# Kernel optimization log

Measured on AMD Instinct MI355X. Metric: run time of the kernel, lower is better.

Reference implementation:

```python
import jax, jax.numpy as jnp
import numpy as np

B, S, D_IN = 2, 2048, 1024
H, DA, DH = 16, 64, 64          # num_heads, attention_dim, head_dim (linear_hidden_dim)
EMBED = 1024
KSIZE = 1


def causal_conv1d(x_bsc, w):
    """x_bsc: (B,S,Cin); w: (Cout,Cin,K). Left-pad K-1 -> causal. Returns (B,Cout,S)."""
    k = w.shape[-1]
    x_bcs = jnp.transpose(x_bsc, (0, 2, 1))
    x_bcs = jnp.pad(x_bcs, ((0, 0), (0, 0), (k - 1, 0)))
    return jax.lax.conv_general_dilated(
        x_bcs, w, window_strides=(1,), padding='VALID',
        dimension_numbers=('NCH', 'OIH', 'NCH'))


def setup_inputs() -> dict:
    key = jax.random.key(0)
    ks = jax.random.split(key, 7)
    x = jax.random.normal(ks[0], (B, S, D_IN), dtype=jnp.float32)
    # causal mask: 1 where attended, 0 where masked (masked_fill where ==0)
    attn_mask = jnp.tril(jnp.ones((S, S), dtype=jnp.int32))[None, None]  # (1,1,S,S)
    wq = 0.02 * jax.random.normal(ks[1], (H * DA, D_IN, KSIZE), dtype=jnp.float32)
    wk = 0.02 * jax.random.normal(ks[2], (H * DA, D_IN, KSIZE), dtype=jnp.float32)
    wv = 0.02 * jax.random.normal(ks[3], (H * DH, D_IN, KSIZE), dtype=jnp.float32)
    w_out = 0.02 * jax.random.normal(ks[4], (EMBED, H * DH), dtype=jnp.float32)
    b_out = 0.02 * jax.random.normal(ks[5], (EMBED,), dtype=jnp.float32)
    return {"x": x, "attn_mask": attn_mask, "wq": wq, "wk": wk, "wv": wv,
            "w_out": w_out, "b_out": b_out}


def reference(x, attn_mask, wq, wk, wv, w_out, b_out):
    b, s, _ = x.shape
    scale = DH ** (-0.5)  # NOTE: torch code scales by head_dim, not attention_dim
    q = causal_conv1d(x, wq)  # (B, H*DA, S)
    k = causal_conv1d(x, wk)  # (B, H*DA, S)
    v = causal_conv1d(x, wv)  # (B, H*DH, S)
    q = q.reshape(b, H, DA, s).transpose(0, 1, 3, 2)  # (B,H,S,DA)
    k = k.reshape(b, H, DA, s).transpose(0, 1, 3, 2)
    v = v.reshape(b, H, DH, s).transpose(0, 1, 3, 2)  # (B,H,S,DH)
    scores = scale * jnp.einsum('bhnd,bhmd->bhnm', q, k)
    scores = jnp.where(attn_mask == 0, -jnp.inf, scores)
    probs = jax.nn.softmax(scores, axis=-1)
    context = jnp.einsum('bhnm,bhmd->bhnd', probs, v)  # (B,H,S,DH)
    context = context.transpose(0, 2, 1, 3).reshape(b, s, H * DH)
    return context @ w_out.T + b_out
```

## Files before the change

kernel.cpp:

```cpp
#include <hip/hip_runtime.h>
#include <math.h>


typedef __bf16 bf16;
typedef __bf16 bf16x8 __attribute__((ext_vector_type(8)));
typedef __bf16 bf16x4 __attribute__((ext_vector_type(4)));
typedef float  f32x4  __attribute__((ext_vector_type(4)));

#define MFMA16(a, b, c) __builtin_amdgcn_mfma_f32_16x16x32_bf16((a), (b), (c), 0, 0, 0)

__device__ __forceinline__ void gll16(const void* g, void* l) {
    __builtin_amdgcn_global_load_lds(
        (__attribute__((address_space(1))) unsigned int*)g,
        (__attribute__((address_space(3))) unsigned int*)l, 16, 0, 0);
}

__global__ __launch_bounds__(256) void cvt_all_kernel(
    const float* __restrict__ x,  const float* __restrict__ wq,
    const float* __restrict__ wk, const float* __restrict__ wv,
    const float* __restrict__ wo,
    bf16* __restrict__ xb,  bf16* __restrict__ wqb, bf16* __restrict__ wkb,
    bf16* __restrict__ wvb, bf16* __restrict__ wob)
{
    #pragma unroll
    for (int k = 0; k < 4; k++) {
        const int blk = blockIdx.x * 4 + k;
        const float* src; bf16* dst; int off; float scale = 1.f;
        if (blk < 4096)      { src = x;  dst = xb;  off = blk * 1024; }
        else if (blk < 5120) { src = wq; dst = wqb; off = (blk - 4096) * 1024;
                               scale = 0.18033688011112042f; }
        else if (blk < 6144) { src = wk; dst = wkb; off = (blk - 5120) * 1024; }
        else if (blk < 7168) { src = wv; dst = wvb; off = (blk - 6144) * 1024; }
        else                 { src = wo; dst = wob; off = (blk - 7168) * 1024; }
        const int i = off + threadIdx.x * 4;
        f32x4 v = *(const f32x4*)(src + i);
        bf16x4 o;
        o[0] = (bf16)(v[0] * scale); o[1] = (bf16)(v[1] * scale);
        o[2] = (bf16)(v[2] * scale); o[3] = (bf16)(v[3] * scale);
        *(bf16x4*)(dst + i) = o;
    }
}

__global__ __launch_bounds__(256, 3) void qkv_mfma_kernel(
    const bf16* __restrict__ xb, const bf16* __restrict__ wqb,
    const bf16* __restrict__ wkb, const bf16* __restrict__ wvb,
    bf16* __restrict__ Qb, bf16* __restrict__ Kb, bf16* __restrict__ Vtb)
{
    __shared__ bf16 As[2][128 * 32];
    __shared__ bf16 Bs[2][128 * 32];
    const int lin = blockIdx.x + 32 * blockIdx.y;
    const int xcd = lin & 7, lid = lin >> 3;
    const int rem = xcd * 96 + lid;
    const int mt = rem & 31;
    const int nt = rem >> 5;
    const int which = nt >> 3;
    const bf16* Wm = (which == 0) ? wqb : (which == 1) ? wkb : wvb;

    const int t = threadIdx.x;
    const int w = t >> 6, lane = t & 63, quad = lane >> 4, l16 = lane & 15;
    const int wm = (w >> 1) * 64, wn = (w & 1) * 64;
    const int srow = lane >> 2;
    const int scol = ((lane & 3) ^ ((lane >> 3) & 3)) * 8;
    const int gx = (l16 >> 1) & 3;

    const bf16* Ab = xb + ((size_t)(mt * 128) + srow) * 1024;
    const bf16* Bb = Wm + ((size_t)((nt & 7) * 128) + srow) * 1024;

    f32x4 acc[4][4];
    #pragma unroll
    for (int i = 0; i < 4; i++)
        #pragma unroll
        for (int j = 0; j < 4; j++)
            #pragma unroll
            for (int r = 0; r < 4; r++) acc[i][j][r] = 0.f;

    gll16(Ab + (size_t)(w * 16) * 1024 + scol,       As[0] + w * 512);
    gll16(Ab + (size_t)((w + 4) * 16) * 1024 + scol, As[0] + (w + 4) * 512);
    gll16(Bb + (size_t)(w * 16) * 1024 + scol,       Bs[0] + w * 512);
    gll16(Bb + (size_t)((w + 4) * 16) * 1024 + scol, Bs[0] + (w + 4) * 512);

    for (int it = 0; it < 32; it++) {
        const int cur = it & 1, nxt = cur ^ 1;
        __syncthreads();
        if (it < 31) {
            const int kn = it * 32 + 32;
            gll16(Ab + (size_t)(w * 16) * 1024 + kn + scol,       As[nxt] + w * 512);
            gll16(Ab + (size_t)((w + 4) * 16) * 1024 + kn + scol, As[nxt] + (w + 4) * 512);
            gll16(Bb + (size_t)(w * 16) * 1024 + kn + scol,       Bs[nxt] + w * 512);
            gll16(Bb + (size_t)((w + 4) * 16) * 1024 + kn + scol, Bs[nxt] + (w + 4) * 512);
        }
        bf16x8 af[4], bfr[4];
        #pragma unroll
        for (int i = 0; i < 4; i++)
            af[i] = *(const bf16x8*)&As[cur][(wm + i * 16 + l16) * 32 +
                                             (quad ^ gx) * 8];
        #pragma unroll
        for (int j = 0; j < 4; j++)
            bfr[j] = *(const bf16x8*)&Bs[cur][(wn + j * 16 + l16) * 32 +
                                              (quad ^ gx) * 8];
        #pragma unroll
        for (int i = 0; i < 4; i++)
            #pragma unroll
            for (int j = 0; j < 4; j++)
                acc[i][j] = MFMA16(af[i], bfr[j], acc[i][j]);
    }

    const int nbase = (nt & 7) * 128 + wn;
    if (which == 2) {
        #pragma unroll
        for (int i = 0; i < 4; i++) {
            const int m0 = mt * 128 + wm + i * 16 + quad * 4;
            const int bb = m0 >> 11, s0 = m0 & 2047;
            #pragma unroll
            for (int j = 0; j < 4; j++) {
                const int n = nbase + j * 16 + l16;
                const int h = n >> 6, d = n & 63;
                bf16x4 pk;
                #pragma unroll
                for (int r = 0; r < 4; r++) pk[r] = (bf16)acc[i][j][r];
                *(bf16x4*)&Vtb[(((size_t)(bb * 16 + h)) * 64 + d) * 2048 + s0] = pk;
            }
        }
    } else {
        bf16* Out = (which == 0) ? Qb : Kb;
        #pragma unroll
        for (int i = 0; i < 4; i++) {
            #pragma unroll
            for (int r = 0; r < 4; r++) {
                const int m = mt * 128 + wm + i * 16 + quad * 4 + r;
                const int bb = m >> 11, s = m & 2047;
                #pragma unroll
                for (int j = 0; j < 4; j++) {
                    const int n = nbase + j * 16 + l16;
                    const int h = n >> 6, d = n & 63;
                    Out[(((size_t)(bb * 16 + h)) * 2048 + s) * 64 + d] =
                        (bf16)acc[i][j][r];
                }
            }
        }
    }
}

__global__ __launch_bounds__(256, 2) void attn_mfma_kernel(
    const bf16* __restrict__ Qb, const bf16* __restrict__ Kb,
    const bf16* __restrict__ Vtb, bf16* __restrict__ ctxb)
{
    __shared__ bf16 Ks[2][128 * 64];
    __shared__ bf16 Vts[2][64 * 128];
    __shared__ bf16 Pl[4][16 * 128];

    const int id = blockIdx.x;
    const int bh = id & 31;
    const int pr = id >> 5;
    const int qa = pr, qb = 31 - pr;
    const int h = bh & 15, b = bh >> 4;
    const int t = threadIdx.x;
    const int w = t >> 6, lane = t & 63, quad = lane >> 4, l16 = lane & 15;

    const size_t hb = (size_t)(b * 16 + h);
    const bf16* Qh = Qb + hb * (2048 * 64);
    const bf16* Kh = Kb + hb * (2048 * 64);
    const bf16* Vh = Vtb + hb * (64 * 2048);

    bf16x8 qf0[2], qf1[2];
    {
        const bf16* Qr0 = Qh + (size_t)(qa * 64 + w * 16 + l16) * 64;
        qf0[0] = *(const bf16x8*)(Qr0 + quad * 8);
        qf0[1] = *(const bf16x8*)(Qr0 + 32 + quad * 8);
        const bf16* Qr1 = Qh + (size_t)(qb * 64 + w * 16 + l16) * 64;
        qf1[0] = *(const bf16x8*)(Qr1 + quad * 8);
        qf1[1] = *(const bf16x8*)(Qr1 + 32 + quad * 8);
    }

    bf16x8 ones;
    #pragma unroll
    for (int i = 0; i < 8; i++) ones[i] = (bf16)1.0f;

    f32x4 o0[4], o1[4], l0, l1;
    #pragma unroll
    for (int r = 0; r < 4; r++) { l0[r] = 0.f; l1[r] = 0.f; }
    #pragma unroll
    for (int dt = 0; dt < 4; dt++)
        #pragma unroll
        for (int r = 0; r < 4; r++) { o0[dt][r] = 0.f; o1[dt][r] = 0.f; }

    const int ksr = lane >> 3, ksc = lane & 7;
    const int vsr = lane >> 4, vsc = lane & 15;

    #define STAGE(ktv, buf)                                                   \
        {                                                                     \
            _Pragma("unroll")                                                 \
            for (int j = 0; j < 4; j++) {                                     \
                const int c = 4 * w + j;                                      \
                const int kr = c * 8 + ksr;                                   \
                gll16(Kh + (size_t)((ktv) * 128 + kr) * 64 +                  \
                          ((ksc ^ (kr & 7)) * 8),                             \
                      Ks[buf] + c * 512);                                     \
                const int vr = c * 4 + vsr;                                   \
                gll16(Vh + (size_t)vr * 2048 + (ktv) * 128 +                  \
                          ((vsc ^ (vr & 15)) * 8),                            \
                      Vts[buf] + c * 512);                                    \
            }                                                                 \
        }

    #define ITER(qt64, ktv, diag, qfv, oacc, lacc, cur)                       \
        {                                                                     \
            f32x4 sacc[8];                                                    \
            __builtin_amdgcn_s_setprio(1);                                    \
            _Pragma("unroll")                                                 \
            for (int tt = 0; tt < 8; tt++) {                                  \
                _Pragma("unroll")                                             \
                for (int r = 0; r < 4; r++) sacc[tt][r] = 0.f;                \
                const int krow = tt * 16 + l16;                               \
                bf16x8 kf0 = *(const bf16x8*)&Ks[cur][krow * 64 +             \
                                 ((quad)     ^ (krow & 7)) * 8];              \
                bf16x8 kf1 = *(const bf16x8*)&Ks[cur][krow * 64 +             \
                                 ((quad + 4) ^ (krow & 7)) * 8];              \
                sacc[tt] = MFMA16(kf0, (qfv)[0], sacc[tt]);                   \
                sacc[tt] = MFMA16(kf1, (qfv)[1], sacc[tt]);                   \
            }                                                                 \
            __builtin_amdgcn_s_setprio(0);                                    \
            const int qrow = (qt64) * 64 + w * 16 + l16;                      \
            _Pragma("unroll")                                                 \
            for (int tt = 0; tt < 8; tt++) {                                  \
                bf16x4 pk;                                                    \
                _Pragma("unroll")                                             \
                for (int r = 0; r < 4; r++) {                                 \
                    float p = __builtin_amdgcn_exp2f(sacc[tt][r]);            \
                    if ((diag) && ((ktv) * 128 + tt * 16 + quad * 4 + r) > qrow) \
                        p = 0.f;                                              \
                    pk[r] = (bf16)p;                                          \
                }                                                             \
                const int cs = (tt * 2 + (quad >> 1)) ^ l16;                  \
                *(bf16x4*)&Pl[w][l16 * 128 + cs * 8 + (quad & 1) * 4] = pk;   \
            }                                                                 \
            bf16x8 ap[4];                                                     \
            __builtin_amdgcn_s_setprio(1);                                    \
            _Pragma("unroll")                                                 \
            for (int u = 0; u < 4; u++) {                                     \
                ap[u] = *(const bf16x8*)&Pl[w][l16 * 128 +                    \
                             ((quad + 4 * u) ^ l16) * 8];                     \
                (lacc) = MFMA16(ap[u], ones, (lacc));                         \
            }                                                                 \
            _Pragma("unroll")                                                 \
            for (int dt = 0; dt < 4; dt++) {                                  \
                const int drow = dt * 16 + l16;                               \
                _Pragma("unroll")                                             \
                for (int u = 0; u < 4; u++) {                                 \
                    bf16x8 bv = *(const bf16x8*)&Vts[cur][drow * 128 +        \
                                     ((4 * u + quad) ^ (drow & 15)) * 8];     \
                    (oacc)[dt] = MFMA16(ap[u], bv, (oacc)[dt]);               \
                }                                                             \
            }                                                                 \
            __builtin_amdgcn_s_setprio(0);                                    \
        }

    const int na = (qa >> 1) + 1;
    STAGE(0, 0);

    for (int v = 0; v < 17; v++) {
        const int cur = v & 1, nxt = cur ^ 1;
        __syncthreads();
        if (v < 16) {
            const int vn = v + 1;
            const int ktn = (vn < na) ? vn : vn - na;
            STAGE(ktn, nxt);
        }
        if (v < na) {
            ITER(qa, v, (v == na - 1), qf0, o0, l0, cur);
        } else {
            const int kt = v - na;
            ITER(qb, kt, (v == 16), qf1, o1, l1, cur);
        }
    }
    #undef STAGE
    #undef ITER

    #pragma unroll
    for (int r = 0; r < 4; r++) {
        const float inv0 = 1.f / l0[r];
        const int s0 = qa * 64 + w * 16 + quad * 4 + r;
        const float inv1 = 1.f / l1[r];
        const int s1 = qb * 64 + w * 16 + quad * 4 + r;
        #pragma unroll
        for (int dt = 0; dt < 4; dt++) {
            ctxb[((size_t)(b * 2048 + s0)) * 1024 + h * 64 + dt * 16 + l16] =
                (bf16)(o0[dt][r] * inv0);
            ctxb[((size_t)(b * 2048 + s1)) * 1024 + h * 64 + dt * 16 + l16] =
                (bf16)(o1[dt][r] * inv1);
        }
    }
}

__global__ __launch_bounds__(256, 3) void oproj_mfma_kernel(
    const bf16* __restrict__ ctxb, const bf16* __restrict__ wob,
    const float* __restrict__ b_out, float* __restrict__ out)
{
    __shared__ bf16 As[2][64 * 64];
    __shared__ bf16 Bs[2][128 * 64];
    const int mt = blockIdx.x;
    const int nt = blockIdx.y;
    const int t = threadIdx.x;
    const int w = t >> 6, lane = t & 63, quad = lane >> 4, l16 = lane & 15;
    const int srow8 = lane >> 3;
    const int scg = ((lane & 7) ^ srow8) * 8;

    const int wrow = (w >> 1) * 32;
    const int wcol = (w & 1) * 64;

    const bf16* Ab = ctxb + (size_t)(mt * 64) * 1024;
    const bf16* Bb = wob + (size_t)(nt * 128) * 1024;

    f32x4 acc[2][4];
    #pragma unroll
    for (int i = 0; i < 2; i++)
        #pragma unroll
        for (int j = 0; j < 4; j++)
            #pragma unroll
            for (int r = 0; r < 4; r++) acc[i][j][r] = 0.f;

    #define OSTG(buf, kk)                                                     \
        {                                                                     \
            gll16(Ab + (size_t)(w * 8 + srow8) * 1024 + (kk) + scg,           \
                  As[buf] + w * 512);                                         \
            gll16(Ab + (size_t)((w + 4) * 8 + srow8) * 1024 + (kk) + scg,     \
                  As[buf] + (w + 4) * 512);                                   \
            _Pragma("unroll")                                                 \
            for (int c = 0; c < 4; c++) {                                     \
                const int ch = w + 4 * c;                                     \
                gll16(Bb + (size_t)(ch * 8 + srow8) * 1024 + (kk) + scg,      \
                      Bs[buf] + ch * 512);                                    \
            }                                                                 \
        }

    OSTG(0, 0);

    for (int it = 0; it < 16; it++) {
        const int cur = it & 1, nxt = cur ^ 1;
        __syncthreads();
        if (it < 15) { OSTG(nxt, it * 64 + 64); }
        bf16x8 af[2][2], bfv[4][2];
        #pragma unroll
        for (int i = 0; i < 2; i++) {
            const int ro = wrow + i * 16 + l16;
            af[i][0] = *(const bf16x8*)&As[cur][ro * 64 + ((quad)     ^ (ro & 7)) * 8];
            af[i][1] = *(const bf16x8*)&As[cur][ro * 64 + ((quad + 4) ^ (ro & 7)) * 8];
        }
        #pragma unroll
        for (int j = 0; j < 4; j++) {
            const int ro = wcol + j * 16 + l16;
            bfv[j][0] = *(const bf16x8*)&Bs[cur][ro * 64 + ((quad)     ^ (ro & 7)) * 8];
            bfv[j][1] = *(const bf16x8*)&Bs[cur][ro * 64 + ((quad + 4) ^ (ro & 7)) * 8];
        }
        #pragma unroll
        for (int i = 0; i < 2; i++)
            #pragma unroll
            for (int j = 0; j < 4; j++) {
                acc[i][j] = MFMA16(af[i][0], bfv[j][0], acc[i][j]);
                acc[i][j] = MFMA16(af[i][1], bfv[j][1], acc[i][j]);
            }
    }
    #undef OSTG

    #pragma unroll
    for (int i = 0; i < 2; i++)
        #pragma unroll
        for (int j = 0; j < 4; j++)
            #pragma unroll
            for (int r = 0; r < 4; r++) {
                const int m = mt * 64 + wrow + i * 16 + quad * 4 + r;
                const int n = nt * 128 + wcol + j * 16 + l16;
                out[(size_t)m * 1024 + n] = acc[i][j][r] + b_out[n];
            }
}

extern "C" void kernel_launch(void* const* d_in, const int* in_sizes, int n_in,
                              void* d_out, int out_size, void* d_ws, size_t ws_size,
                              hipStream_t stream)
{
    const float* x     = (const float*)d_in[0];
    const float* wq    = (const float*)d_in[2];
    const float* wk    = (const float*)d_in[3];
    const float* wv    = (const float*)d_in[4];
    const float* w_out = (const float*)d_in[5];
    const float* b_out = (const float*)d_in[6];
    float* out = (float*)d_out;

    char* ws = (char*)d_ws;
    bf16* xb   = (bf16*)(ws);
    bf16* wqb  = (bf16*)(ws + (8u  << 20));
    bf16* wkb  = (bf16*)(ws + (10u << 20));
    bf16* wvb  = (bf16*)(ws + (12u << 20));
    bf16* wob  = (bf16*)(ws + (14u << 20));
    bf16* Qb   = (bf16*)(ws + (16u << 20));
    bf16* Kb   = (bf16*)(ws + (24u << 20));
    bf16* Vtb  = (bf16*)(ws + (32u << 20));
    bf16* ctxb = (bf16*)(ws + (40u << 20));

    cvt_all_kernel<<<2048, 256, 0, stream>>>(x, wq, wk, wv, w_out,
                                             xb, wqb, wkb, wvb, wob);
    qkv_mfma_kernel<<<dim3(32, 24), 256, 0, stream>>>(xb, wqb, wkb, wvb, Qb, Kb, Vtb);
    attn_mfma_kernel<<<512, 256, 0, stream>>>(Qb, Kb, Vtb, ctxb);
    oproj_mfma_kernel<<<dim3(64, 8), 256, 0, stream>>>(ctxb, wob, b_out, out);
}
```

Baseline: 178.4 us.

## Rework attention with 32x32 MFMA, register-resident P, and per-tile causal scheduling

The attention kernel moves from 16x16x32 to 32x32x16 bf16 MFMA. Each wave now owns 32 query rows, and each block owns one 128-row query tile. The softmax probabilities are packed with v_cvt_pk_bf16 and rearranged across lanes with v_permlane32_swap, so they stay in registers instead of going through a shared-memory scratch buffer. Row sums become scalar adds plus one cross-half shuffle, replacing the MFMA against a ones vector. The old pairing of a short and a long query tile in one block is dropped. Load balance now relies on launch order, with the second half of the grid running tiles in reverse. That can leave tail imbalance and adds register pressure from the 16-wide accumulators.

Result: no change. 177.5 us, median of 2 (-0.5%).

```diff
diff --git a/kernel.cpp b/kernel.cpp
--- a/kernel.cpp
+++ b/kernel.cpp
@@ -6,13 +6,21 @@
 typedef __bf16 bf16x8 __attribute__((ext_vector_type(8)));
 typedef __bf16 bf16x4 __attribute__((ext_vector_type(4)));
 typedef float  f32x4  __attribute__((ext_vector_type(4)));
+typedef float  f32x16 __attribute__((ext_vector_type(16)));
 
 #define MFMA16(a, b, c) __builtin_amdgcn_mfma_f32_16x16x32_bf16((a), (b), (c), 0, 0, 0)
+#define MFMA32(a, b, c) __builtin_amdgcn_mfma_f32_32x32x16_bf16((a), (b), (c), 0, 0, 0)
 
 __device__ __forceinline__ void gll16(const void* g, void* l) {
     __builtin_amdgcn_global_load_lds(
         (__attribute__((address_space(1))) unsigned int*)g,
         (__attribute__((address_space(3))) unsigned int*)l, 16, 0, 0);
+}
+
+__device__ __forceinline__ unsigned int cvt_pk_bf16(float lo, float hi) {
+    unsigned int r;
+    asm("v_cvt_pk_bf16_f32 %0, %1, %2" : "=v"(r) : "v"(lo), "v"(hi));
+    return r;
 }
 
 __global__ __launch_bounds__(256) void cvt_all_kernel(
@@ -147,42 +155,33 @@
 {
     __shared__ bf16 Ks[2][128 * 64];
     __shared__ bf16 Vts[2][64 * 128];
-    __shared__ bf16 Pl[4][16 * 128];
-
-    const int id = blockIdx.x;
-    const int bh = id & 31;
-    const int pr = id >> 5;
-    const int qa = pr, qb = 31 - pr;
+
+    const int g = blockIdx.x;
+    const int base = g & 255;
+    const int bh = base & 31;
+    const int tp = base >> 5;
+    const int t  = (g < 256) ? tp : 15 - tp;
     const int h = bh & 15, b = bh >> 4;
-    const int t = threadIdx.x;
-    const int w = t >> 6, lane = t & 63, quad = lane >> 4, l16 = lane & 15;
+    const int tid = threadIdx.x;
+    const int w = tid >> 6, lane = tid & 63;
+    const int l32 = lane & 31, hv = lane >> 5;
 
     const size_t hb = (size_t)(b * 16 + h);
     const bf16* Qh = Qb + hb * (2048 * 64);
     const bf16* Kh = Kb + hb * (2048 * 64);
     const bf16* Vh = Vtb + hb * (64 * 2048);
 
-    bf16x8 qf0[2], qf1[2];
-    {
-        const bf16* Qr0 = Qh + (size_t)(qa * 64 + w * 16 + l16) * 64;
-        qf0[0] = *(const bf16x8*)(Qr0 + quad * 8);
-        qf0[1] = *(const bf16x8*)(Qr0 + 32 + quad * 8);
-        const bf16* Qr1 = Qh + (size_t)(qb * 64 + w * 16 + l16) * 64;
-        qf1[0] = *(const bf16x8*)(Qr1 + quad * 8);
-        qf1[1] = *(const bf16x8*)(Qr1 + 32 + quad * 8);
-    }
-
-    bf16x8 ones;
-    #pragma unroll
-    for (int i = 0; i < 8; i++) ones[i] = (bf16)1.0f;
-
-    f32x4 o0[4], o1[4], l0, l1;
-    #pragma unroll
-    for (int r = 0; r < 4; r++) { l0[r] = 0.f; l1[r] = 0.f; }
-    #pragma unroll
-    for (int dt = 0; dt < 4; dt++)
-        #pragma unroll
-        for (int r = 0; r < 4; r++) { o0[dt][r] = 0.f; o1[dt][r] = 0.f; }
+    const int qrow = t * 128 + w * 32 + l32;
+
+    bf16x8 qf[4];
+    #pragma unroll
+    for (int ks = 0; ks < 4; ks++)
+        qf[ks] = *(const bf16x8*)(Qh + (size_t)qrow * 64 + ks * 16 + hv * 8);
+
+    f32x16 o0, o1, zero16;
+    #pragma unroll
+    for (int r = 0; r < 16; r++) { o0[r] = 0.f; o1[r] = 0.f; zero16[r] = 0.f; }
+    float lacc = 0.f;
 
     const int ksr = lane >> 3, ksc = lane & 7;
     const int vsr = lane >> 4, vsc = lane & 15;
@@ -203,92 +202,81 @@
             }                                                                 \
         }
 
-    #define ITER(qt64, ktv, diag, qfv, oacc, lacc, cur)                       \
-        {                                                                     \
-            f32x4 sacc[8];                                                    \
-            __builtin_amdgcn_s_setprio(1);                                    \
-            _Pragma("unroll")                                                 \
-            for (int tt = 0; tt < 8; tt++) {                                  \
-                _Pragma("unroll")                                             \
-                for (int r = 0; r < 4; r++) sacc[tt][r] = 0.f;                \
-                const int krow = tt * 16 + l16;                               \
-                bf16x8 kf0 = *(const bf16x8*)&Ks[cur][krow * 64 +             \
-                                 ((quad)     ^ (krow & 7)) * 8];              \
-                bf16x8 kf1 = *(const bf16x8*)&Ks[cur][krow * 64 +             \
-                                 ((quad + 4) ^ (krow & 7)) * 8];              \
-                sacc[tt] = MFMA16(kf0, (qfv)[0], sacc[tt]);                   \
-                sacc[tt] = MFMA16(kf1, (qfv)[1], sacc[tt]);                   \
-            }                                                                 \
-            __builtin_amdgcn_s_setprio(0);                                    \
-            const int qrow = (qt64) * 64 + w * 16 + l16;                      \
-            _Pragma("unroll")                                                 \
-            for (int tt = 0; tt < 8; tt++) {                                  \
-                bf16x4 pk;                                                    \
-                _Pragma("unroll")                                             \
-                for (int r = 0; r < 4; r++) {                                 \
-                    float p = __builtin_amdgcn_exp2f(sacc[tt][r]);            \
-                    if ((diag) && ((ktv) * 128 + tt * 16 + quad * 4 + r) > qrow) \
-                        p = 0.f;                                              \
-                    pk[r] = (bf16)p;                                          \
-                }                                                             \
-                const int cs = (tt * 2 + (quad >> 1)) ^ l16;                  \
-                *(bf16x4*)&Pl[w][l16 * 128 + cs * 8 + (quad & 1) * 4] = pk;   \
-            }                                                                 \
-            bf16x8 ap[4];                                                     \
-            __builtin_amdgcn_s_setprio(1);                                    \
-            _Pragma("unroll")                                                 \
-            for (int u = 0; u < 4; u++) {                                     \
-                ap[u] = *(const bf16x8*)&Pl[w][l16 * 128 +                    \
-                             ((quad + 4 * u) ^ l16) * 8];                     \
-                (lacc) = MFMA16(ap[u], ones, (lacc));                         \
-            }                                                                 \
-            _Pragma("unroll")                                                 \
-            for (int dt = 0; dt < 4; dt++) {                                  \
-                const int drow = dt * 16 + l16;                               \
-                _Pragma("unroll")                                             \
-                for (int u = 0; u < 4; u++) {                                 \
-                    bf16x8 bv = *(const bf16x8*)&Vts[cur][drow * 128 +        \
-                                     ((4 * u + quad) ^ (drow & 15)) * 8];     \
-                    (oacc)[dt] = MFMA16(ap[u], bv, (oacc)[dt]);               \
-                }                                                             \
-            }                                                                 \
-            __builtin_amdgcn_s_setprio(0);                                    \
-        }
-
-    const int na = (qa >> 1) + 1;
     STAGE(0, 0);
 
-    for (int v = 0; v < 17; v++) {
-        const int cur = v & 1, nxt = cur ^ 1;
+    for (int v = 0; v <= t; v++) {
+        const int cur = v & 1;
         __syncthreads();
-        if (v < 16) {
-            const int vn = v + 1;
-            const int ktn = (vn < na) ? vn : vn - na;
-            STAGE(ktn, nxt);
-        }
-        if (v < na) {
-            ITER(qa, v, (v == na - 1), qf0, o0, l0, cur);
-        } else {
-            const int kt = v - na;
-            ITER(qb, kt, (v == 16), qf1, o1, l1, cur);
-        }
+        if (v < t) STAGE(v + 1, cur ^ 1);
+        const bool diag = (v == t);
+
+        f32x16 sacc[4];
+        const int rowx = l32 & 7;
+        __builtin_amdgcn_s_setprio(1);
+        #pragma unroll
+        for (int c = 0; c < 4; c++) {
+            const int key = c * 32 + l32;
+            bf16x8 kf0 = *(const bf16x8*)&Ks[cur][key * 64 + ((hv ^ rowx) * 8)];
+            sacc[c] = MFMA32(kf0, qf[0], zero16);
+            #pragma unroll
+            for (int ks = 1; ks < 4; ks++) {
+                bf16x8 kf = *(const bf16x8*)&Ks[cur][key * 64 +
+                                (((ks * 2 + hv) ^ rowx) * 8)];
+                sacc[c] = MFMA32(kf, qf[ks], sacc[c]);
+            }
+        }
+        __builtin_amdgcn_s_setprio(0);
+
+        #pragma unroll
+        for (int c = 0; c < 4; c++) {
+            #pragma unroll
+            for (int r = 0; r < 16; r++) {
+                float p = __builtin_amdgcn_exp2f(sacc[c][r]);
+                if (diag) {
+                    const int key = v * 128 + c * 32 + (r & 3) + 8 * (r >> 2)
+                                    + 4 * hv;
+                    if (key > qrow) p = 0.f;
+                }
+                sacc[c][r] = p;
+                lacc += p;
+            }
+        }
+
+        __builtin_amdgcn_s_setprio(1);
+        #pragma unroll
+        for (int c = 0; c < 4; c++) {
+            #pragma unroll
+            for (int hh = 0; hh < 2; hh++) {
+                unsigned int W0 = cvt_pk_bf16(sacc[c][8 * hh + 0], sacc[c][8 * hh + 1]);
+                unsigned int W1 = cvt_pk_bf16(sacc[c][8 * hh + 2], sacc[c][8 * hh + 3]);
+                unsigned int W2 = cvt_pk_bf16(sacc[c][8 * hh + 4], sacc[c][8 * hh + 5]);
+                unsigned int W3 = cvt_pk_bf16(sacc[c][8 * hh + 6], sacc[c][8 * hh + 7]);
+                asm volatile("v_permlane32_swap_b32 %0, %1" : "+v"(W0), "+v"(W2));
+                asm volatile("v_permlane32_swap_b32 %0, %1" : "+v"(W1), "+v"(W3));
+                union { unsigned int u[4]; bf16x8 v8; } fu;
+                fu.u[0] = W0; fu.u[1] = W1; fu.u[2] = W2; fu.u[3] = W3;
+                const int kc = c * 2 + hh;
+                const int gA = ((kc * 2 + hv) ^ (l32 & 15)) * 8;
+                bf16x8 bv0 = *(const bf16x8*)&Vts[cur][l32 * 128 + gA];
+                bf16x8 bv1 = *(const bf16x8*)&Vts[cur][(l32 + 32) * 128 + gA];
+                o0 = MFMA32(fu.v8, bv0, o0);
+                o1 = MFMA32(fu.v8, bv1, o1);
+            }
+        }
+        __builtin_amdgcn_s_setprio(0);
     }
     #undef STAGE
-    #undef ITER
-
-    #pragma unroll
-    for (int r = 0; r < 4; r++) {
-        const float inv0 = 1.f / l0[r];
-        const int s0 = qa * 64 + w * 16 + quad * 4 + r;
-        const float inv1 = 1.f / l1[r];
-        const int s1 = qb * 64 + w * 16 + quad * 4 + r;
-        #pragma unroll
-        for (int dt = 0; dt < 4; dt++) {
-            ctxb[((size_t)(b * 2048 + s0)) * 1024 + h * 64 + dt * 16 + l16] =
-                (bf16)(o0[dt][r] * inv0);
-            ctxb[((size_t)(b * 2048 + s1)) * 1024 + h * 64 + dt * 16 + l16] =
-                (bf16)(o1[dt][r] * inv1);
-        }
+
+    const float lfull = lacc + __shfl_xor(lacc, 32);
+    const float inv = 1.f / lfull;
+    #pragma unroll
+    for (int r = 0; r < 16; r++) {
+        const int rloc = (r & 3) + 8 * (r >> 2) + 4 * hv;
+        const float invr = __shfl(inv, rloc);
+        const int srow = t * 128 + w * 32 + rloc;
+        const size_t rowoff = ((size_t)(b * 2048 + srow)) * 1024 + h * 64;
+        ctxb[rowoff + l32]      = (bf16)(o0[r] * invr);
+        ctxb[rowoff + 32 + l32] = (bf16)(o1[r] * invr);
     }
 }
 
```
